# Kernel optimization log

Hardware: AMD Instinct MI355X
Metric: run time of the kernel (lower is better)

Reference implementation:

```python
import jax, jax.numpy as jnp
import numpy as np

N = 100000
E = 640000
C = 128
NEG_SLOPE = 0.2


def _param(key, shape, scale=0.1):
    return jax.random.normal(key, shape, dtype=jnp.float32) * scale


def setup_inputs() -> dict:
    key = jax.random.key(0)
    ks = jax.random.split(key, 20)
    edge_index = jax.random.randint(ks[0], (2, E), 0, N, dtype=jnp.int32)
    emb = jax.random.normal(ks[1], (N, C), dtype=jnp.float32)  # node_embeddings.weight, a=1.0 normal
    d = {"edge_index": edge_index, "emb": emb}
    # per-layer GATv2Conv params: lin_l (W,b), lin_r (W,b), att vector, residual lin (no bias), out bias
    names = ["Wl", "bl", "Wr", "br", "att", "Wres", "bias"]
    shapes = [(C, C), (C,), (C, C), (C,), (C,), (C, C), (C,)]
    i = 2
    for layer in (1, 2):
        for nm, sh in zip(names, shapes):
            d[f"l{layer}_{nm}"] = _param(ks[i], sh)
            i += 1
    return d


def gatv2_layer(x, Wl, bl, Wr, br, att, Wres, bias, src, dst):
    # x: [N,C]; src/dst: [E+N] (self loops included)
    xl = x @ Wl.T + bl                       # source-side transform [N,C]
    xr = x @ Wr.T + br                       # target-side transform [N,C]
    m = jax.nn.leaky_relu(xl[src] + xr[dst], NEG_SLOPE)  # [E',C]
    e = m @ att                               # attention logits [E']
    emax = jax.ops.segment_max(e, dst, num_segments=N)
    ex = jnp.exp(e - emax[dst])
    denom = jax.ops.segment_sum(ex, dst, num_segments=N)
    alpha = ex / denom[dst]                   # segment softmax over incoming edges
    out = jax.ops.segment_sum(alpha[:, None] * xl[src], dst, num_segments=N)
    return out + x @ Wres.T + bias            # residual + bias


def reference(edge_index, emb,
              l1_Wl, l1_bl, l1_Wr, l1_br, l1_att, l1_Wres, l1_bias,
              l2_Wl, l2_bl, l2_Wr, l2_br, l2_att, l2_Wres, l2_bias):
    loops = jnp.arange(N, dtype=edge_index.dtype)
    src = jnp.concatenate([edge_index[0], loops])
    dst = jnp.concatenate([edge_index[1], loops])
    h = gatv2_layer(emb, l1_Wl, l1_bl, l1_Wr, l1_br, l1_att, l1_Wres, l1_bias, src, dst)
    h = jax.nn.relu(h)
    out = gatv2_layer(h, l2_Wl, l2_bl, l2_Wr, l2_br, l2_att, l2_Wres, l2_bias, src, dst)
    return out
```

## Files before the change

kernel.cpp:

```cpp
#include <hip/hip_runtime.h>
#include <math.h>

#define N_NODES 100000
#define N_EDGES 640000
#define C 128
#define CAP 32
#define TILES_PB 3
#define N_TILES ((N_NODES + 63) / 64)

typedef __attribute__((ext_vector_type(8))) short short8;
typedef __attribute__((ext_vector_type(4))) float floatx4;
typedef __attribute__((ext_vector_type(2))) float float2v;
typedef unsigned int uint;
typedef unsigned short ushort;

__device__ __forceinline__ ushort f2bf(float f) {
    union { float f; uint u; } v; v.f = f;
    uint r = v.u + 0x7fffu + ((v.u >> 16) & 1u);
    return (ushort)(r >> 16);
}
__device__ __forceinline__ float2v upk2(uint u) {
    union { uint i; float f; } lo, hi;
    lo.i = u << 16; hi.i = u & 0xffff0000u;
    float2v r; r.x = lo.f; r.y = hi.f; return r;
}
__device__ __forceinline__ float2v fabs2(float2v v) {
    union { float2v f; uint u[2]; } a; a.f = v;
    a.u[0] &= 0x7fffffffu; a.u[1] &= 0x7fffffffu; return a.f;
}
__device__ __forceinline__ float2v fma2(float2v a, float2v b, float2v c) {
    return __builtin_elementwise_fma(a, b, c);
}

__global__ void prep_kernel(const float* __restrict__ w0, const float* __restrict__ w1,
                            const float* __restrict__ w2, const float* __restrict__ w3,
                            const float* __restrict__ w4, const float* __restrict__ w5,
                            ushort* __restrict__ wb, int* __restrict__ cnt) {
    const int bid = blockIdx.x;
    if (bid < 48) {
        int t = bid * 256 + threadIdx.x;
        int m = t >> 11;
        int off = (t & 2047) * 8;
        const float* src = (m == 0) ? w0 : (m == 1) ? w1 : (m == 2) ? w2
                          : (m == 3) ? w3 : (m == 4) ? w4 : w5;
        float4 v0 = *(const float4*)(src + off);
        float4 v1 = *(const float4*)(src + off + 4);
        ushort tmp[8];
        tmp[0] = f2bf(v0.x); tmp[1] = f2bf(v0.y); tmp[2] = f2bf(v0.z); tmp[3] = f2bf(v0.w);
        tmp[4] = f2bf(v1.x); tmp[5] = f2bf(v1.y); tmp[6] = f2bf(v1.z); tmp[7] = f2bf(v1.w);
        *(uint4*)(wb + (size_t)m * 16384 + off) = *(uint4*)tmp;
    } else {
        int idx = (bid - 48) * 256 + threadIdx.x;
        if (idx < N_NODES) cnt[idx] = 0;
    }
}

__global__ void build_kernel(const int* __restrict__ ei, int* __restrict__ cnt,
                             int* __restrict__ colsrc) {
    int i = blockIdx.x * 256 + threadIdx.x;
    if (i >= N_EDGES) return;
    int d = ei[N_EDGES + i];
    int s = ei[i];
    int slot = atomicAdd(&cnt[d], 1);
    if (slot < CAP) colsrc[(size_t)d * CAP + slot] = s;
}

template <int IN_F32, int RES_F32>
__global__ __launch_bounds__(512)
void gemm3_pipe(const void* __restrict__ xin,
                const ushort* __restrict__ wb,
                const float* __restrict__ bl, const float* __restrict__ br,
                const float* __restrict__ bres,
                ushort* __restrict__ xl, ushort* __restrict__ xr,
                void* __restrict__ res) {
    __shared__ ushort xs[2][64][136];
    const int tid = threadIdx.x;
    const int wave = tid >> 6, lane = tid & 63;
    const int quad = lane >> 4, l16 = lane & 15;
    const int col = wave * 16 + l16;
    const int node = tid >> 3;
    const int kc = (tid & 7) * 16;

    short8 bfr[3][4];
    #pragma unroll
    for (int ws = 0; ws < 3; ++ws)
        #pragma unroll
        for (int ks = 0; ks < 4; ++ks)
            bfr[ws][ks] = *(const short8*)(wb + (size_t)ws * 16384 + (size_t)col * 128 + ks * 32 + quad * 8);

    const float bias[3] = { bl[col], br[col], bres[col] };

    const int t0 = blockIdx.x * TILES_PB;

    auto load_tile = [&](int tile, ushort* tmp) {
        const int n = tile * 64 + node;
        if (n < N_NODES) {
            if (IN_F32) {
                const float* src = (const float*)xin + (size_t)n * C + kc;
                float4 v[4];
                #pragma unroll
                for (int i = 0; i < 4; ++i) v[i] = ((const float4*)src)[i];
                #pragma unroll
                for (int i = 0; i < 4; ++i) {
                    tmp[i * 4 + 0] = f2bf(v[i].x); tmp[i * 4 + 1] = f2bf(v[i].y);
                    tmp[i * 4 + 2] = f2bf(v[i].z); tmp[i * 4 + 3] = f2bf(v[i].w);
                }
            } else {
                const ushort* src = (const ushort*)xin + (size_t)n * C + kc;
                *(uint4*)&tmp[0] = *(const uint4*)src;
                *(uint4*)&tmp[8] = *(const uint4*)(src + 8);
            }
        } else {
            #pragma unroll
            for (int i = 0; i < 16; ++i) tmp[i] = 0;
        }
    };

    ushort stg[16];
    load_tile(t0, stg);
    *(uint4*)&xs[0][node][kc]     = *(uint4*)&stg[0];
    *(uint4*)&xs[0][node][kc + 8] = *(uint4*)&stg[8];

    for (int i = 0; i < TILES_PB; ++i) {
        const int tile = t0 + i;
        __syncthreads();

        const bool more = (i + 1 < TILES_PB);
        if (more) load_tile(tile + 1, stg);

        floatx4 acc[4][3];
        #pragma unroll
        for (int rt = 0; rt < 4; ++rt)
            #pragma unroll
            for (int ws = 0; ws < 3; ++ws)
                acc[rt][ws] = (floatx4){0.f, 0.f, 0.f, 0.f};

        #pragma unroll
        for (int rt = 0; rt < 4; ++rt) {
            short8 a[4];
            #pragma unroll
            for (int ks = 0; ks < 4; ++ks)
                a[ks] = *(const short8*)&xs[i & 1][rt * 16 + l16][ks * 32 + quad * 8];
            #pragma unroll
            for (int ws = 0; ws < 3; ++ws)
                #pragma unroll
                for (int ks = 0; ks < 4; ++ks)
                    acc[rt][ws] = __builtin_amdgcn_mfma_f32_16x16x32_bf16(a[ks], bfr[ws][ks], acc[rt][ws], 0, 0, 0);
        }

        if (more) {
            *(uint4*)&xs[(i + 1) & 1][node][kc]     = *(uint4*)&stg[0];
            *(uint4*)&xs[(i + 1) & 1][node][kc + 8] = *(uint4*)&stg[8];
        }

        const int n0 = tile * 64;
        #pragma unroll
        for (int ws = 0; ws < 3; ++ws)
            #pragma unroll
            for (int rt = 0; rt < 4; ++rt)
                #pragma unroll
                for (int r = 0; r < 4; ++r) {
                    int row = n0 + rt * 16 + quad * 4 + r;
                    if (row < N_NODES) {
                        float val = acc[rt][ws][r] + bias[ws];
                        if (ws == 0)      xl[(size_t)row * C + col] = f2bf(val);
                        else if (ws == 1) xr[(size_t)row * C + col] = f2bf(val);
                        else if (RES_F32) ((float*)res)[(size_t)row * C + col] = val;
                        else              ((ushort*)res)[(size_t)row * C + col] = f2bf(val);
                    }
                }
    }
}

template <int OUT_BF16, int RELU, int RES_F32>
__global__ __launch_bounds__(256)
void node_kernel(const ushort* __restrict__ xl, const ushort* __restrict__ xr,
                 const float* __restrict__ att, const int* __restrict__ cnt,
                 const int* __restrict__ colsrc,
                 const void* __restrict__ resin, void* __restrict__ outp) {
    const int tid = threadIdx.x;
    const int gl = tid & 15;
    const int base_c = gl * 8;
    const int d = blockIdx.x * 16 + (tid >> 4);

    float4 at0 = *(const float4*)(att + base_c);
    float4 at1 = *(const float4*)(att + base_c + 4);
    float2v a06[4], a04[4];
    a06[0] = (float2v){0.6f * at0.x, 0.6f * at0.y};
    a06[1] = (float2v){0.6f * at0.z, 0.6f * at0.w};
    a06[2] = (float2v){0.6f * at1.x, 0.6f * at1.y};
    a06[3] = (float2v){0.6f * at1.z, 0.6f * at1.w};
    a04[0] = (float2v){0.4f * at0.x, 0.4f * at0.y};
    a04[1] = (float2v){0.4f * at0.z, 0.4f * at0.w};
    a04[2] = (float2v){0.4f * at1.x, 0.4f * at1.y};
    a04[3] = (float2v){0.4f * at1.z, 0.4f * at1.w};

    uint4 uxr = *(const uint4*)(xr + (size_t)d * C + base_c);
    float2v xr2[4] = { upk2(uxr.x), upk2(uxr.y), upk2(uxr.z), upk2(uxr.w) };

    const int deg0 = cnt[d];
    const int deg = (deg0 < CAP) ? deg0 : CAP;
    const int* cs = colsrc + (size_t)d * CAP;
    const int nch = (deg + 3) >> 2;

    uint4 selfraw = *(const uint4*)(xl + (size_t)d * C + base_c);

    int4 sA = make_int4(d, d, d, d);
    if (deg > 0) sA = *(const int4*)cs;
    sA.x = (0 < deg) ? sA.x : d;
    sA.y = (1 < deg) ? sA.y : d;
    sA.z = (2 < deg) ? sA.z : d;
    sA.w = (3 < deg) ? sA.w : d;
    uint4 R0 = *(const uint4*)(xl + (size_t)sA.x * C + base_c);
    uint4 R1 = *(const uint4*)(xl + (size_t)sA.y * C + base_c);
    uint4 R2 = *(const uint4*)(xl + (size_t)sA.z * C + base_c);
    uint4 R3 = *(const uint4*)(xl + (size_t)sA.w * C + base_c);
    int4 sB = make_int4(d, d, d, d);
    if (deg > 4) sB = *(const int4*)(cs + 4);

    float S;
    float2v O2[4];

    {
        float2v xv[4] = { upk2(selfraw.x), upk2(selfraw.y), upk2(selfraw.z), upk2(selfraw.w) };
        float2v m0 = xv[0] + xr2[0];
        float2v m1 = xv[1] + xr2[1];
        float2v m2 = xv[2] + xr2[2];
        float2v m3 = xv[3] + xr2[3];
        float2v pa = fma2(a06[0], m0, a04[0] * fabs2(m0));
        float2v pb = fma2(a06[1], m1, a04[1] * fabs2(m1));
        pa = fma2(a06[2], m2, fma2(a04[2], fabs2(m2), pa));
        pb = fma2(a06[3], m3, fma2(a04[3], fabs2(m3), pb));
        pa += pb;
        float p = pa.x + pa.y;
        #pragma unroll
        for (int off = 1; off < 16; off <<= 1) p += __shfl_xor(p, off, 64);
        const float w = __expf(p);
        S = w;
        float2v w2 = (float2v){w, w};
        #pragma unroll
        for (int j = 0; j < 4; ++j) O2[j] = w2 * xv[j];
    }

    for (int c = 0; c < nch; ++c) {
        const uint4 c0 = R0, c1 = R1, c2 = R2, c3 = R3;

        const int nb = (c + 1) * 4;
        int4 sN = sB;
        sN.x = (nb + 0 < deg) ? sN.x : d;
        sN.y = (nb + 1 < deg) ? sN.y : d;
        sN.z = (nb + 2 < deg) ? sN.z : d;
        sN.w = (nb + 3 < deg) ? sN.w : d;
        const int bb = (c + 2) * 4;
        if (bb < deg) sB = *(const int4*)(cs + bb);

        R0 = *(const uint4*)(xl + (size_t)sN.x * C + base_c);
        R1 = *(const uint4*)(xl + (size_t)sN.y * C + base_c);
        R2 = *(const uint4*)(xl + (size_t)sN.z * C + base_c);
        R3 = *(const uint4*)(xl + (size_t)sN.w * C + base_c);

        const int e0 = c * 4;
        const uint4 cur[4] = { c0, c1, c2, c3 };
        #pragma unroll
        for (int j = 0; j < 4; ++j) {
            float2v xv[4] = { upk2(cur[j].x), upk2(cur[j].y), upk2(cur[j].z), upk2(cur[j].w) };
            float2v m0 = xv[0] + xr2[0];
            float2v m1 = xv[1] + xr2[1];
            float2v m2 = xv[2] + xr2[2];
            float2v m3 = xv[3] + xr2[3];
            float2v pa = fma2(a06[0], m0, a04[0] * fabs2(m0));
            float2v pb = fma2(a06[1], m1, a04[1] * fabs2(m1));
            pa = fma2(a06[2], m2, fma2(a04[2], fabs2(m2), pa));
            pb = fma2(a06[3], m3, fma2(a04[3], fabs2(m3), pb));
            pa += pb;
            float p = pa.x + pa.y;
            #pragma unroll
            for (int off = 1; off < 16; off <<= 1) p += __shfl_xor(p, off, 64);
            const float w = (e0 + j < deg) ? __expf(p) : 0.f;
            S += w;
            float2v w2 = (float2v){w, w};
            #pragma unroll
            for (int k = 0; k < 4; ++k) O2[k] = fma2(w2, xv[k], O2[k]);
        }
    }

    const float inv = 1.f / S;
    float2v rs[4];
    if (RES_F32) {
        const float* rp = (const float*)resin + (size_t)d * C + base_c;
        float4 q0 = *(const float4*)rp;
        float4 q1 = *(const float4*)(rp + 4);
        rs[0] = (float2v){q0.x, q0.y}; rs[1] = (float2v){q0.z, q0.w};
        rs[2] = (float2v){q1.x, q1.y}; rs[3] = (float2v){q1.z, q1.w};
    } else {
        uint4 urs = *(const uint4*)((const ushort*)resin + (size_t)d * C + base_c);
        rs[0] = upk2(urs.x); rs[1] = upk2(urs.y); rs[2] = upk2(urs.z); rs[3] = upk2(urs.w);
    }
    float2v iv = (float2v){inv, inv};
    float r[8];
    #pragma unroll
    for (int j = 0; j < 4; ++j) {
        float2v rr = fma2(O2[j], iv, rs[j]);
        if (RELU) { rr.x = fmaxf(rr.x, 0.f); rr.y = fmaxf(rr.y, 0.f); }
        r[2 * j] = rr.x; r[2 * j + 1] = rr.y;
    }
    if (OUT_BF16) {
        ushort tmp[8];
        #pragma unroll
        for (int c2 = 0; c2 < 8; ++c2) tmp[c2] = f2bf(r[c2]);
        *((uint4*)((ushort*)outp + (size_t)d * C + base_c)) = *(uint4*)tmp;
    } else {
        float* op = (float*)outp + (size_t)d * C + base_c;
        *(float4*)op       = make_float4(r[0], r[1], r[2], r[3]);
        *(float4*)(op + 4) = make_float4(r[4], r[5], r[6], r[7]);
    }
}

extern "C" void kernel_launch(void* const* d_in, const int* in_sizes, int n_in,
                              void* d_out, int out_size, void* d_ws, size_t ws_size,
                              hipStream_t stream) {
    const int*   ei  = (const int*)d_in[0];
    const float* emb = (const float*)d_in[1];
    const float* L1[7];
    const float* L2[7];
    for (int i = 0; i < 7; ++i) L1[i] = (const float*)d_in[2 + i];
    for (int i = 0; i < 7; ++i) L2[i] = (const float*)d_in[9 + i];
    float* out = (float*)d_out;

    const size_t NC = (size_t)N_NODES * C;
    ushort* xl  = (ushort*)d_ws;
    ushort* xr  = xl + NC;
    ushort* h   = xr + NC;
    ushort* wb  = h + NC;
    int* cnt    = (int*)(wb + 6 * 16384);
    int* colsrc = cnt + N_NODES;

    prep_kernel<<<48 + (N_NODES + 255) / 256, 256, 0, stream>>>(
        L1[0], L1[2], L1[5], L2[0], L2[2], L2[5], wb, cnt);
    build_kernel<<<(N_EDGES + 255) / 256, 256, 0, stream>>>(ei, cnt, colsrc);

    const int gblocks = (N_TILES + TILES_PB - 1) / TILES_PB;
    const int nblocks = N_NODES / 16;

    gemm3_pipe<1, 0><<<gblocks, 512, 0, stream>>>(emb, wb, L1[1], L1[3], L1[6], xl, xr, h);
    node_kernel<1, 1, 0><<<nblocks, 256, 0, stream>>>(xl, xr, L1[4], cnt, colsrc, h, h);

    gemm3_pipe<0, 1><<<gblocks, 512, 0, stream>>>(h, wb + 3 * 16384, L2[1], L2[3], L2[6], xl, xr, out);
    node_kernel<0, 0, 1><<<nblocks, 256, 0, stream>>>(xl, xr, L2[4], cnt, colsrc, out, out);
}
```

Before: 313.2 us.

## Sort nodes by degree per block, use DPP reductions and 32-bit gather addressing

Each block loads the 16 node degrees into shared memory and ranks them so that wavefronts process nodes of similar degree together, which is meant to reduce divergence in the edge loop. The 16-lane butterfly shuffle reduction is replaced with DPP row operations (quad permutes plus row shifts), avoiding LDS-based shuffles. Gather addresses are computed with 32-bit arithmetic instead of size_t. This adds two block barriers and a small ranking loop per block, and the DPP row_shr pattern relies on bound_ctrl zero-fill and must still leave the full group sum in every lane that uses it.

```diff
diff --git a/kernel.cpp b/kernel.cpp
--- a/kernel.cpp
+++ b/kernel.cpp
@@ -30,6 +30,16 @@
 }
 __device__ __forceinline__ float2v fma2(float2v a, float2v b, float2v c) {
     return __builtin_elementwise_fma(a, b, c);
+}
+
+__device__ __forceinline__ float grp16_sum(float p) {
+    union { float f; int i; } u, t;
+    u.f = p;
+    t.i = __builtin_amdgcn_update_dpp(0, u.i, 0xB1, 0xf, 0xf, true);  u.f += t.f;
+    t.i = __builtin_amdgcn_update_dpp(0, u.i, 0x4E, 0xf, 0xf, true);  u.f += t.f;
+    t.i = __builtin_amdgcn_update_dpp(0, u.i, 0x124, 0xf, 0xf, true); u.f += t.f;
+    t.i = __builtin_amdgcn_update_dpp(0, u.i, 0x128, 0xf, 0xf, true); u.f += t.f;
+    return u.f;
 }
 
 __global__ void prep_kernel(const float* __restrict__ w0, const float* __restrict__ w1,
@@ -178,10 +188,29 @@
                  const float* __restrict__ att, const int* __restrict__ cnt,
                  const int* __restrict__ colsrc,
                  const void* __restrict__ resin, void* __restrict__ outp) {
+    __shared__ int sdeg[16];
+    __shared__ short smap[16];
     const int tid = threadIdx.x;
+
+    if (tid < 16) sdeg[tid] = cnt[blockIdx.x * 16 + tid];
+    __syncthreads();
+    if (tid < 16) {
+        const int my = sdeg[tid];
+        int rank = 0;
+        #pragma unroll
+        for (int j = 0; j < 16; ++j) {
+            const int dj = sdeg[j];
+            rank += (int)((dj > my) | ((dj == my) & (j < tid)));
+        }
+        smap[rank] = (short)tid;
+    }
+    __syncthreads();
+
     const int gl = tid & 15;
     const int base_c = gl * 8;
-    const int d = blockIdx.x * 16 + (tid >> 4);
+    const int lidx = (int)smap[tid >> 4];
+    const int d = blockIdx.x * 16 + lidx;
+    const int deg0 = sdeg[lidx];
 
     float4 at0 = *(const float4*)(att + base_c);
     float4 at1 = *(const float4*)(att + base_c + 4);
@@ -198,12 +227,15 @@
     uint4 uxr = *(const uint4*)(xr + (size_t)d * C + base_c);
     float2v xr2[4] = { upk2(uxr.x), upk2(uxr.y), upk2(uxr.z), upk2(uxr.w) };
 
-    const int deg0 = cnt[d];
     const int deg = (deg0 < CAP) ? deg0 : CAP;
     const int* cs = colsrc + (size_t)d * CAP;
     const int nch = (deg + 3) >> 2;
 
     uint4 selfraw = *(const uint4*)(xl + (size_t)d * C + base_c);
+
+    auto xlrow = [&](int s) -> const uint4* {
+        return (const uint4*)(xl + (((uint)s << 7) + (uint)base_c));
+    };
 
     int4 sA = make_int4(d, d, d, d);
     if (deg > 0) sA = *(const int4*)cs;
@@ -211,10 +243,10 @@
     sA.y = (1 < deg) ? sA.y : d;
     sA.z = (2 < deg) ? sA.z : d;
     sA.w = (3 < deg) ? sA.w : d;
-    uint4 R0 = *(const uint4*)(xl + (size_t)sA.x * C + base_c);
-    uint4 R1 = *(const uint4*)(xl + (size_t)sA.y * C + base_c);
-    uint4 R2 = *(const uint4*)(xl + (size_t)sA.z * C + base_c);
-    uint4 R3 = *(const uint4*)(xl + (size_t)sA.w * C + base_c);
+    uint4 R0 = *xlrow(sA.x);
+    uint4 R1 = *xlrow(sA.y);
+    uint4 R2 = *xlrow(sA.z);
+    uint4 R3 = *xlrow(sA.w);
     int4 sB = make_int4(d, d, d, d);
     if (deg > 4) sB = *(const int4*)(cs + 4);
 
@@ -232,9 +264,7 @@
         pa = fma2(a06[2], m2, fma2(a04[2], fabs2(m2), pa));
         pb = fma2(a06[3], m3, fma2(a04[3], fabs2(m3), pb));
         pa += pb;
-        float p = pa.x + pa.y;
-        #pragma unroll
-        for (int off = 1; off < 16; off <<= 1) p += __shfl_xor(p, off, 64);
+        float p = grp16_sum(pa.x + pa.y);
         const float w = __expf(p);
         S = w;
         float2v w2 = (float2v){w, w};
@@ -254,10 +284,10 @@
         const int bb = (c + 2) * 4;
         if (bb < deg) sB = *(const int4*)(cs + bb);
 
-        R0 = *(const uint4*)(xl + (size_t)sN.x * C + base_c);
-        R1 = *(const uint4*)(xl + (size_t)sN.y * C + base_c);
-        R2 = *(const uint4*)(xl + (size_t)sN.z * C + base_c);
-        R3 = *(const uint4*)(xl + (size_t)sN.w * C + base_c);
+        R0 = *xlrow(sN.x);
+        R1 = *xlrow(sN.y);
+        R2 = *xlrow(sN.z);
+        R3 = *xlrow(sN.w);
 
         const int e0 = c * 4;
         const uint4 cur[4] = { c0, c1, c2, c3 };
@@ -273,9 +303,7 @@
             pa = fma2(a06[2], m2, fma2(a04[2], fabs2(m2), pa));
             pb = fma2(a06[3], m3, fma2(a04[3], fabs2(m3), pb));
             pa += pb;
-            float p = pa.x + pa.y;
-            #pragma unroll
-            for (int off = 1; off < 16; off <<= 1) p += __shfl_xor(p, off, 64);
+            float p = grp16_sum(pa.x + pa.y);
             const float w = (e0 + j < deg) ? __expf(p) : 0.f;
             S += w;
             float2v w2 = (float2v){w, w};
```

New measurement: 311.1 us. No clear change (-0.6%).
